# Kernel tuning notes

Hardware: AMD Instinct MI355X
Metric: run time of the kernel (lower is better)

The kernel has to match this reference:

```python
import jax, jax.numpy as jnp
import numpy as np

IN_F, OUT_F, TASK_D, RANK, HID = 1024, 1024, 256, 8, 64
ALPHA = 8.0
SCALING = ALPHA / RANK  # 1.0


def setup_inputs() -> dict:
    key = jax.random.key(0)
    ks = jax.random.split(key, 12)
    s = 0.02
    return {
        "x": jax.random.normal(ks[0], (4, 2048, IN_F), dtype=jnp.float32),
        "base_out": jax.random.normal(ks[1], (4, 2048, OUT_F), dtype=jnp.float32),
        "task_emb": jax.random.normal(ks[2], (4, TASK_D), dtype=jnp.float32),
        # gen_a MLP: Linear(task_dim->hid) + GELU + Linear(hid->out*r)
        "Wa1": jax.random.normal(ks[3], (HID, TASK_D), dtype=jnp.float32) * s,
        "ba1": jnp.zeros((HID,), dtype=jnp.float32),
        "Wa2": jax.random.normal(ks[4], (OUT_F * RANK, HID), dtype=jnp.float32) * s,
        "ba2": jnp.zeros((OUT_F * RANK,), dtype=jnp.float32),
        # gen_b MLP: Linear(task_dim->hid) + GELU + Linear(hid->r*in)
        "Wb1": jax.random.normal(ks[5], (HID, TASK_D), dtype=jnp.float32) * s,
        "bb1": jnp.zeros((HID,), dtype=jnp.float32),
        "Wb2": jax.random.normal(ks[6], (RANK * IN_F, HID), dtype=jnp.float32) * s,
        "bb2": jnp.zeros((RANK * IN_F,), dtype=jnp.float32),
    }


def reference(x, base_out, task_emb, Wa1, ba1, Wa2, ba2, Wb1, bb1, Wb2, bb2):
    lead = x.shape[:-1]
    x2d = x.reshape(-1, IN_F)                      # (b_eff, in)
    b_eff = x2d.shape[0]
    # broadcast task_emb to b_eff rows (repeat + trim, as in torch)
    B = task_emb.shape[0]
    reps = (b_eff + B - 1) // B
    task_eff = jnp.tile(task_emb, (reps, 1))[:b_eff]  # (b_eff, task_dim)

    gelu = lambda t: jax.nn.gelu(t, approximate=False)
    h_a = gelu(task_eff @ Wa1.T + ba1)
    vec_a = h_a @ Wa2.T + ba2                      # (b_eff, out*r)
    h_b = gelu(task_eff @ Wb1.T + bb1)
    vec_b = h_b @ Wb2.T + bb2                      # (b_eff, r*in)

    a = vec_a.reshape(b_eff, OUT_F, RANK)
    b = vec_b.reshape(b_eff, RANK, IN_F)

    # dropout p=0 (eval): x passes through
    tmp = jnp.einsum('bi,bri->br', x2d, b)         # (b_eff, r)
    y_delta = jnp.einsum('br,bor->bo', tmp, a)     # (b_eff, out)
    y = base_out.reshape(-1, OUT_F) + SCALING * y_delta
    return y.reshape(*lead, OUT_F)
```

## Files before the change

kernel.cpp:

```cpp
#include <hip/hip_runtime.h>
#include <math.h>

#define IN_F   1024
#define OUT_F  1024
#define TASK_D 256
#define RANK   8
#define HID    64

__device__ __forceinline__ float gelu_exact(float v) {
    return 0.5f * v * (1.0f + erff(v * 0.70710678118654752f));
}

__global__ __launch_bounds__(256) void gen_kernel(
    const float* __restrict__ task_emb,
    const float* __restrict__ Wa1, const float* __restrict__ ba1,
    const float* __restrict__ Wa2, const float* __restrict__ ba2,
    const float* __restrict__ Wb1, const float* __restrict__ bb1,
    const float* __restrict__ Wb2, const float* __restrict__ bb2,
    float* __restrict__ vec_a, float* __restrict__ vec_b)
{
    const int gen   = blockIdx.x >> 5;
    const int obase = (blockIdx.x & 31) * 256;
    const float* __restrict__ W1  = gen ? Wb1 : Wa1;
    const float* __restrict__ b1  = gen ? bb1 : ba1;
    const float* __restrict__ W2  = gen ? Wb2 : Wa2;
    const float* __restrict__ b2  = gen ? bb2 : ba2;
    float* __restrict__ vec       = gen ? vec_b : vec_a;

    __shared__ float hs[4][HID];
    {
        const int t = threadIdx.x >> 6;
        const int j = threadIdx.x & 63;
        const float4* te = (const float4*)(task_emb + t * TASK_D);
        const float4* w  = (const float4*)(W1 + j * TASK_D);
        float acc = 0.f;
        #pragma unroll
        for (int d = 0; d < TASK_D / 4; ++d) {
            float4 a = te[d], b = w[d];
            acc += a.x * b.x + a.y * b.y + a.z * b.z + a.w * b.w;
        }
        hs[t][j] = gelu_exact(acc + b1[j]);
    }
    __syncthreads();

    const int o = obase + threadIdx.x;
    const float4* w2 = (const float4*)(W2 + (size_t)o * HID);
    float acc0 = 0.f, acc1 = 0.f, acc2 = 0.f, acc3 = 0.f;
    #pragma unroll
    for (int k = 0; k < HID / 4; ++k) {
        float4 w = w2[k];
        const int kb = 4 * k;
        acc0 += hs[0][kb] * w.x + hs[0][kb+1] * w.y + hs[0][kb+2] * w.z + hs[0][kb+3] * w.w;
        acc1 += hs[1][kb] * w.x + hs[1][kb+1] * w.y + hs[1][kb+2] * w.z + hs[1][kb+3] * w.w;
        acc2 += hs[2][kb] * w.x + hs[2][kb+1] * w.y + hs[2][kb+2] * w.z + hs[2][kb+3] * w.w;
        acc3 += hs[3][kb] * w.x + hs[3][kb+1] * w.y + hs[3][kb+2] * w.z + hs[3][kb+3] * w.w;
    }
    const float bb = b2[o];
    vec[0 * 8192 + o] = acc0 + bb;
    vec[1 * 8192 + o] = acc1 + bb;
    vec[2 * 8192 + o] = acc2 + bb;
    vec[3 * 8192 + o] = acc3 + bb;
}

__global__ __launch_bounds__(256) void apply_kernel(
    const float* __restrict__ x, const float* __restrict__ base_out,
    const float* __restrict__ vec_a, const float* __restrict__ vec_b,
    float* __restrict__ out)
{
    const int wave = threadIdx.x >> 6;
    const int lane = threadIdx.x & 63;
    const int row  = blockIdx.x * 4 + wave;
    const int t    = row & 3;

    const float* __restrict__ xr = x + (size_t)row * IN_F;
    const float* __restrict__ bt = vec_b + (size_t)t * (RANK * IN_F);

    float acc[RANK];
    #pragma unroll
    for (int r = 0; r < RANK; ++r) acc[r] = 0.f;

    #pragma unroll
    for (int c = 0; c < IN_F / 256; ++c) {
        const int k = c * 256 + lane * 4;
        const float4 xv = *(const float4*)(xr + k);
        #pragma unroll
        for (int r = 0; r < RANK; ++r) {
            const float4 bv = *(const float4*)(bt + r * IN_F + k);
            acc[r] += xv.x * bv.x + xv.y * bv.y + xv.z * bv.z + xv.w * bv.w;
        }
    }

    #pragma unroll
    for (int off = 32; off > 0; off >>= 1) {
        #pragma unroll
        for (int r = 0; r < RANK; ++r)
            acc[r] += __shfl_xor(acc[r], off, 64);
    }

    const float* __restrict__ at = vec_a + (size_t)t * (OUT_F * RANK);
    const float* __restrict__ br = base_out + (size_t)row * OUT_F;
    float* __restrict__ orow     = out + (size_t)row * OUT_F;

    #pragma unroll
    for (int c = 0; c < OUT_F / 256; ++c) {
        const int o = c * 256 + lane * 4;
        const float4 bo = *(const float4*)(br + o);
        float res[4];
        const float bof[4] = { bo.x, bo.y, bo.z, bo.w };
        #pragma unroll
        for (int q = 0; q < 4; ++q) {
            const float4 a0 = *(const float4*)(at + (size_t)(o + q) * RANK);
            const float4 a1 = *(const float4*)(at + (size_t)(o + q) * RANK + 4);
            res[q] = bof[q]
                   + acc[0] * a0.x + acc[1] * a0.y + acc[2] * a0.z + acc[3] * a0.w
                   + acc[4] * a1.x + acc[5] * a1.y + acc[6] * a1.z + acc[7] * a1.w;
        }
        float4 rv = { res[0], res[1], res[2], res[3] };
        *(float4*)(orow + o) = rv;
    }
}

extern "C" void kernel_launch(void* const* d_in, const int* in_sizes, int n_in,
                              void* d_out, int out_size, void* d_ws, size_t ws_size,
                              hipStream_t stream) {
    const float* x        = (const float*)d_in[0];
    const float* base_out = (const float*)d_in[1];
    const float* task_emb = (const float*)d_in[2];
    const float* Wa1      = (const float*)d_in[3];
    const float* ba1      = (const float*)d_in[4];
    const float* Wa2      = (const float*)d_in[5];
    const float* ba2      = (const float*)d_in[6];
    const float* Wb1      = (const float*)d_in[7];
    const float* bb1      = (const float*)d_in[8];
    const float* Wb2      = (const float*)d_in[9];
    const float* bb2      = (const float*)d_in[10];
    float* out   = (float*)d_out;

    float* vec_a = (float*)d_ws;
    float* vec_b = vec_a + 4 * OUT_F * RANK;

    const int b_eff = in_sizes[0] / IN_F;

    gen_kernel<<<64, 256, 0, stream>>>(task_emb, Wa1, ba1, Wa2, ba2,
                                       Wb1, bb1, Wb2, bb2, vec_a, vec_b);
    apply_kernel<<<b_eff / 4, 256, 0, stream>>>(x, base_out, vec_a, vec_b, out);
}
```

Baseline: 169.3 us.

## Transpose vec_a layout, stage vec_b in LDS, group same-task rows per block

The generator kernel now runs on 256 blocks, with four threads splitting each output's hidden-dim dot product and combining them through shuffles. It writes vec_a in a rank-major transposed layout so the apply kernel can read it with coalesced float4 loads. The apply kernel groups rows that share the same task into one block, copies that task's 32KB vec_b into shared memory, and handles two rows per wave so the A loads are reused. In exchange the apply kernel uses 32KB of LDS per block, which may limit occupancy, and it launches half as many blocks.

```diff
diff --git a/kernel.cpp b/kernel.cpp
--- a/kernel.cpp
+++ b/kernel.cpp
@@ -17,20 +17,19 @@
     const float* __restrict__ Wa2, const float* __restrict__ ba2,
     const float* __restrict__ Wb1, const float* __restrict__ bb1,
     const float* __restrict__ Wb2, const float* __restrict__ bb2,
-    float* __restrict__ vec_a, float* __restrict__ vec_b)
+    float* __restrict__ vec_a_t, float* __restrict__ vec_b)
 {
-    const int gen   = blockIdx.x >> 5;
-    const int obase = (blockIdx.x & 31) * 256;
-    const float* __restrict__ W1  = gen ? Wb1 : Wa1;
-    const float* __restrict__ b1  = gen ? bb1 : ba1;
-    const float* __restrict__ W2  = gen ? Wb2 : Wa2;
-    const float* __restrict__ b2  = gen ? bb2 : ba2;
-    float* __restrict__ vec       = gen ? vec_b : vec_a;
+    const int gen = blockIdx.x >> 7;
+    const int blk = blockIdx.x & 127;
+    const float* __restrict__ W1 = gen ? Wb1 : Wa1;
+    const float* __restrict__ b1 = gen ? bb1 : ba1;
+    const float* __restrict__ W2 = gen ? Wb2 : Wa2;
+    const float* __restrict__ b2 = gen ? bb2 : ba2;
 
     __shared__ float hs[4][HID];
     {
-        const int t = threadIdx.x >> 6;
-        const int j = threadIdx.x & 63;
+        const int j = threadIdx.x >> 2;
+        const int t = threadIdx.x & 3;
         const float4* te = (const float4*)(task_emb + t * TASK_D);
         const float4* w  = (const float4*)(W1 + j * TASK_D);
         float acc = 0.f;
@@ -43,80 +42,121 @@
     }
     __syncthreads();
 
-    const int o = obase + threadIdx.x;
-    const float4* w2 = (const float4*)(W2 + (size_t)o * HID);
+    const int lrow = threadIdx.x >> 2;
+    const int q    = threadIdx.x & 3;
+    const int o    = blk * 64 + lrow;
+
+    const float4* w2 = (const float4*)(W2 + (size_t)o * HID + q * 16);
     float acc0 = 0.f, acc1 = 0.f, acc2 = 0.f, acc3 = 0.f;
     #pragma unroll
-    for (int k = 0; k < HID / 4; ++k) {
+    for (int k = 0; k < 4; ++k) {
         float4 w = w2[k];
-        const int kb = 4 * k;
+        const int kb = q * 16 + k * 4;
         acc0 += hs[0][kb] * w.x + hs[0][kb+1] * w.y + hs[0][kb+2] * w.z + hs[0][kb+3] * w.w;
         acc1 += hs[1][kb] * w.x + hs[1][kb+1] * w.y + hs[1][kb+2] * w.z + hs[1][kb+3] * w.w;
         acc2 += hs[2][kb] * w.x + hs[2][kb+1] * w.y + hs[2][kb+2] * w.z + hs[2][kb+3] * w.w;
         acc3 += hs[3][kb] * w.x + hs[3][kb+1] * w.y + hs[3][kb+2] * w.z + hs[3][kb+3] * w.w;
     }
-    const float bb = b2[o];
-    vec[0 * 8192 + o] = acc0 + bb;
-    vec[1 * 8192 + o] = acc1 + bb;
-    vec[2 * 8192 + o] = acc2 + bb;
-    vec[3 * 8192 + o] = acc3 + bb;
+    #pragma unroll
+    for (int off = 1; off <= 2; off <<= 1) {
+        acc0 += __shfl_xor(acc0, off, 64);
+        acc1 += __shfl_xor(acc1, off, 64);
+        acc2 += __shfl_xor(acc2, off, 64);
+        acc3 += __shfl_xor(acc3, off, 64);
+    }
+    if (q == 0) {
+        const float bb = b2[o];
+        float v[4] = { acc0 + bb, acc1 + bb, acc2 + bb, acc3 + bb };
+        if (gen == 0) {
+            const int oo = o >> 3, r = o & 7;
+            #pragma unroll
+            for (int t = 0; t < 4; ++t)
+                vec_a_t[t * (RANK * OUT_F) + r * OUT_F + oo] = v[t];
+        } else {
+            #pragma unroll
+            for (int t = 0; t < 4; ++t)
+                vec_b[t * (RANK * IN_F) + o] = v[t];
+        }
+    }
 }
 
 __global__ __launch_bounds__(256) void apply_kernel(
     const float* __restrict__ x, const float* __restrict__ base_out,
-    const float* __restrict__ vec_a, const float* __restrict__ vec_b,
+    const float* __restrict__ vec_a_t, const float* __restrict__ vec_b,
     float* __restrict__ out)
 {
+    const int t    = blockIdx.x & 3;
+    const int g    = blockIdx.x >> 2;
     const int wave = threadIdx.x >> 6;
     const int lane = threadIdx.x & 63;
-    const int row  = blockIdx.x * 4 + wave;
-    const int t    = row & 3;
 
-    const float* __restrict__ xr = x + (size_t)row * IN_F;
-    const float* __restrict__ bt = vec_b + (size_t)t * (RANK * IN_F);
+    __shared__ float bs[RANK * IN_F];
+    {
+        const float4* src = (const float4*)(vec_b + (size_t)t * (RANK * IN_F));
+        float4* dst = (float4*)bs;
+        #pragma unroll
+        for (int i = 0; i < 8; ++i)
+            dst[threadIdx.x + 256 * i] = src[threadIdx.x + 256 * i];
+    }
+    __syncthreads();
 
-    float acc[RANK];
-    #pragma unroll
-    for (int r = 0; r < RANK; ++r) acc[r] = 0.f;
+    const int jbase = g * 8 + wave * 2;
+    float tmp[2][RANK];
 
     #pragma unroll
-    for (int c = 0; c < IN_F / 256; ++c) {
-        const int k = c * 256 + lane * 4;
-        const float4 xv = *(const float4*)(xr + k);
+    for (int i = 0; i < 2; ++i) {
+        const int row = t + 4 * (jbase + i);
+        const float* __restrict__ xr = x + (size_t)row * IN_F;
+        float4 xv[4];
         #pragma unroll
-        for (int r = 0; r < RANK; ++r) {
-            const float4 bv = *(const float4*)(bt + r * IN_F + k);
-            acc[r] += xv.x * bv.x + xv.y * bv.y + xv.z * bv.z + xv.w * bv.w;
+        for (int c = 0; c < 4; ++c)
+            xv[c] = *(const float4*)(xr + c * 256 + lane * 4);
+
+        float acc[RANK];
+        #pragma unroll
+        for (int r = 0; r < RANK; ++r) acc[r] = 0.f;
+        #pragma unroll
+        for (int c = 0; c < 4; ++c) {
+            const int k = c * 256 + lane * 4;
+            #pragma unroll
+            for (int r = 0; r < RANK; ++r) {
+                const float4 bv = *(const float4*)(bs + r * IN_F + k);
+                acc[r] += xv[c].x * bv.x + xv[c].y * bv.y + xv[c].z * bv.z + xv[c].w * bv.w;
+            }
         }
+        #pragma unroll
+        for (int off = 32; off > 0; off >>= 1) {
+            #pragma unroll
+            for (int r = 0; r < RANK; ++r)
+                acc[r] += __shfl_xor(acc[r], off, 64);
+        }
+        #pragma unroll
+        for (int r = 0; r < RANK; ++r) tmp[i][r] = acc[r];
     }
 
+    const float* __restrict__ at = vec_a_t + (size_t)t * (RANK * OUT_F);
     #pragma unroll
-    for (int off = 32; off > 0; off >>= 1) {
+    for (int c = 0; c < 4; ++c) {
+        const int o = c * 256 + lane * 4;
+        float4 af[RANK];
         #pragma unroll
         for (int r = 0; r < RANK; ++r)
-            acc[r] += __shfl_xor(acc[r], off, 64);
-    }
-
-    const float* __restrict__ at = vec_a + (size_t)t * (OUT_F * RANK);
-    const float* __restrict__ br = base_out + (size_t)row * OUT_F;
-    float* __restrict__ orow     = out + (size_t)row * OUT_F;
-
-    #pragma unroll
-    for (int c = 0; c < OUT_F / 256; ++c) {
-        const int o = c * 256 + lane * 4;
-        const float4 bo = *(const float4*)(br + o);
-        float res[4];
-        const float bof[4] = { bo.x, bo.y, bo.z, bo.w };
+            af[r] = *(const float4*)(at + r * OUT_F + o);
         #pragma unroll
-        for (int q = 0; q < 4; ++q) {
-            const float4 a0 = *(const float4*)(at + (size_t)(o + q) * RANK);
-            const float4 a1 = *(const float4*)(at + (size_t)(o + q) * RANK + 4);
-            res[q] = bof[q]
-                   + acc[0] * a0.x + acc[1] * a0.y + acc[2] * a0.z + acc[3] * a0.w
-                   + acc[4] * a1.x + acc[5] * a1.y + acc[6] * a1.z + acc[7] * a1.w;
+        for (int i = 0; i < 2; ++i) {
+            const int row = t + 4 * (jbase + i);
+            const float4 bo = *(const float4*)(base_out + (size_t)row * OUT_F + o);
+            float4 rv;
+            rv.x = bo.x; rv.y = bo.y; rv.z = bo.z; rv.w = bo.w;
+            #pragma unroll
+            for (int r = 0; r < RANK; ++r) {
+                rv.x += tmp[i][r] * af[r].x;
+                rv.y += tmp[i][r] * af[r].y;
+                rv.z += tmp[i][r] * af[r].z;
+                rv.w += tmp[i][r] * af[r].w;
+            }
+            *(float4*)(out + (size_t)row * OUT_F + o) = rv;
         }
-        float4 rv = { res[0], res[1], res[2], res[3] };
-        *(float4*)(orow + o) = rv;
     }
 }
 
@@ -134,14 +174,14 @@
     const float* bb1      = (const float*)d_in[8];
     const float* Wb2      = (const float*)d_in[9];
     const float* bb2      = (const float*)d_in[10];
-    float* out   = (float*)d_out;
+    float* out = (float*)d_out;
 
-    float* vec_a = (float*)d_ws;
-    float* vec_b = vec_a + 4 * OUT_F * RANK;
+    float* vec_a_t = (float*)d_ws;
+    float* vec_b   = vec_a_t + 4 * RANK * OUT_F;
 
     const int b_eff = in_sizes[0] / IN_F;
 
-    gen_kernel<<<64, 256, 0, stream>>>(task_emb, Wa1, ba1, Wa2, ba2,
-                                       Wb1, bb1, Wb2, bb2, vec_a, vec_b);
-    apply_kernel<<<b_eff / 4, 256, 0, stream>>>(x, base_out, vec_a, vec_b, out);
+    gen_kernel<<<256, 256, 0, stream>>>(task_emb, Wa1, ba1, Wa2, ba2,
+                                        Wb1, bb1, Wb2, bb2, vec_a_t, vec_b);
+    apply_kernel<<<b_eff / 8, 256, 0, stream>>>(x, base_out, vec_a_t, vec_b, out);
 }
```

Result: faster. 137.1 us (-19.0%).
